# Optimization experiments

Measured on AMD Instinct MI355X. Metric: run time of the kernel, lower is better.

Reference implementation:

```python
import jax, jax.numpy as jnp
import numpy as np

LN_EPS = 1e-5

def _ln(x, gamma, beta):
    mu = jnp.mean(x, axis=-1, keepdims=True)
    var = jnp.mean((x - mu) ** 2, axis=-1, keepdims=True)
    return (x - mu) * jax.lax.rsqrt(var + LN_EPS) * gamma + beta

def setup_inputs() -> dict:
    key = jax.random.key(0)
    ks = jax.random.split(key, 16)
    B, T, D_E, D_H, D_T = 64, 1024, 512, 512, 64
    def xavier(k, shape):
        fan_in, fan_out = shape[0], shape[1]
        a = np.sqrt(6.0 / (fan_in + fan_out))
        return jax.random.uniform(k, shape, jnp.float32, -a, a)
    return {
        "inputs": jax.random.normal(ks[0], (B, T, D_E), jnp.float32),
        "embedding": xavier(ks[1], (D_E, D_H)),
        "w_x_0": xavier(ks[2], (D_H, D_H)),
        "w_h_0": xavier(ks[3], (D_H, D_H)),
        "b_0": xavier(ks[4], (1, D_H)),
        "w_x_1": xavier(ks[5], (D_H, D_H)),
        "w_h_1": xavier(ks[6], (D_H, D_H)),
        "b_1": xavier(ks[7], (1, D_H)),
        "w_x_2": xavier(ks[8], (D_H, D_H)),
        "w_h_2": xavier(ks[9], (D_H, D_H)),
        "b_2": xavier(ks[10], (1, D_H)),
        "ln_gamma": jnp.ones((D_H,), jnp.float32),
        "ln_beta": jnp.zeros((D_H,), jnp.float32),
        "clf_w": xavier(ks[11], (D_H, D_T)),
        "clf_b": jnp.zeros((D_T,), jnp.float32),
    }

def reference(inputs, embedding, w_x_0, w_h_0, b_0, w_x_1, w_h_1, b_1,
              w_x_2, w_h_2, b_2, ln_gamma, ln_beta, clf_w, clf_b):
    B, T, _ = inputs.shape
    D_H = embedding.shape[1]
    # Precompute the (input @ embedding) projection for all steps: [T, B, D_H]
    v_all = jnp.einsum('bte,eh->tbh', inputs, embedding)

    def step(carry, v_t):
        h0p, h1p, h2p, _ = carry
        h0 = jnp.tanh(v_t @ w_x_0 + h0p @ w_h_0 + b_0)
        o0 = _ln(h0, ln_gamma, ln_beta)
        h1 = jnp.tanh(o0 @ w_x_1 + h1p @ w_h_1 + b_1)
        o1 = _ln(h1, ln_gamma, ln_beta)
        h2 = jnp.tanh(o1 @ w_x_2 + h2p @ w_h_2 + b_2)
        o2 = _ln(h2, ln_gamma, ln_beta)
        # note: raw h_t (pre-LayerNorm) is what recurs, per the original code
        return (h0, h1, h2, o2), None

    z = jnp.zeros((B, D_H), inputs.dtype)
    (_, _, _, out_2), _ = jax.lax.scan(step, (z, z, z, z), v_all)
    logits = out_2 @ clf_w + clf_b  # [B, D_T]
    return jax.nn.softmax(logits, axis=1)
```

## Files before the change

kernel.cpp:

```cpp
#include <hip/hip_runtime.h>

#define DH 512
#define TT 1024
#define BB 64
#define DT 64
#define RD 4
#define RG 32

typedef _Float16 f16x8 __attribute__((ext_vector_type(8)));
typedef float f32x4 __attribute__((ext_vector_type(4)));

#define ATILE_HALVES  (64 * 65 * 8)
#define ATILE32_HALVES (64 * 33 * 8)

__device__ __forceinline__ f16x8 cload(const _Float16* p) {
  return *(const volatile f16x8*)p;
}
__device__ __forceinline__ void cstore(_Float16* p, f16x8 v) {
  *(volatile f16x8*)p = v;
}


__global__ __launch_bounds__(512) void eprime_kernel(
    const float* __restrict__ emb, const float* __restrict__ wx0,
    float* __restrict__ Ep)
{
  __shared__ float er[DH];
  const int e = blockIdx.x, j = threadIdx.x;
  er[j] = emb[(size_t)e * DH + j];
  __syncthreads();
  float acc = 0.f;
#pragma unroll 8
  for (int k = 0; k < DH; ++k) acc = fmaf(er[k], wx0[(size_t)k * DH + j], acc);
  Ep[(size_t)e * DH + j] = acc;
}

__global__ __launch_bounds__(512) void pack_kernel(
    const float* __restrict__ Ep, const float* __restrict__ wh0,
    const float* __restrict__ wx1, const float* __restrict__ wh1,
    const float* __restrict__ wx2, const float* __restrict__ wh2,
    const float* __restrict__ gamma, _Float16* __restrict__ dst)
{
  __shared__ float Tt[64][65];
  const int m = blockIdx.z, jt = blockIdx.x, kt = blockIdx.y;
  const float* src = (m == 0) ? Ep : (m == 1) ? wh0 : (m == 2) ? wx1
                   : (m == 3) ? wh1 : (m == 4) ? wx2 : wh2;
  const bool fold = (m == 2 || m == 4);
  const int tx = threadIdx.x & 63, ty = threadIdx.x >> 6;
#pragma unroll
  for (int i = 0; i < 8; ++i) {
    const int k = kt * 64 + ty * 8 + i;
    Tt[ty * 8 + i][tx] = src[(size_t)k * DH + jt * 64 + tx];
  }
  __syncthreads();
#pragma unroll
  for (int i = 0; i < 8; ++i) {
    const int j = jt * 64 + ty * 8 + i;
    const int k = kt * 64 + tx;
    float v = Tt[tx][ty * 8 + i];
    if (fold) v *= gamma[k];
    dst[((size_t)m * DH + j) * DH + k] = (_Float16)v;
  }
}

__global__ __launch_bounds__(512) void fold_kernel(
    const float* __restrict__ b0, const float* __restrict__ b1,
    const float* __restrict__ b2, const float* __restrict__ wx1,
    const float* __restrict__ wx2, const float* __restrict__ gamma,
    const float* __restrict__ beta, const float* __restrict__ clfw,
    const float* __restrict__ clfb,
    float* __restrict__ bfold, float* __restrict__ csum,
    float* __restrict__ clfwf, float* __restrict__ clfbf)
{
  const int j = threadIdx.x;
  if (blockIdx.x == 0) {
    bfold[j] = b0[j];
    float s1 = 0, s2 = 0, c1 = 0, c2 = 0;
    for (int k = 0; k < DH; ++k) {
      const float w1 = wx1[(size_t)k * DH + j], w2 = wx2[(size_t)k * DH + j];
      s1 += beta[k] * w1;  s2 += beta[k] * w2;
      c1 += gamma[k] * w1; c2 += gamma[k] * w2;
    }
    bfold[DH + j] = b1[j] + s1;
    bfold[2 * DH + j] = b2[j] + s2;
    csum[j] = c1; csum[DH + j] = c2;
  } else {
    for (int idx = j; idx < DH * DT; idx += 512) {
      const int k = idx >> 6, d = idx & 63;
      clfwf[idx] = gamma[k] * clfw[(size_t)k * DT + d];
    }
    if (j < DT) {
      float sb = clfb[j];
      for (int k = 0; k < DH; ++k) sb += beta[k] * clfw[(size_t)k * DT + j];
      clfbf[j] = sb;
    }
  }
}

__global__ __launch_bounds__(512, 1) void vgemm_kernel(
    const float* __restrict__ x, const _Float16* __restrict__ Bt,
    _Float16* __restrict__ v)
{
  const int t = blockIdx.x;
  const int tid = threadIdx.x, l = tid & 63, w = tid >> 6;
  __shared__ __align__(16) _Float16 A[ATILE_HALVES];
  {
    const int row = tid >> 3, part = tid & 7;
    const float4* sp = (const float4*)(x + ((size_t)row * TT + t) * DH);
#pragma unroll
    for (int i = 0; i < 8; ++i) {
      const int ks = i * 8 + part;
      const float4 a = sp[ks * 2], b = sp[ks * 2 + 1];
      f16x8 vv;
      vv[0] = (_Float16)a.x; vv[1] = (_Float16)a.y; vv[2] = (_Float16)a.z; vv[3] = (_Float16)a.w;
      vv[4] = (_Float16)b.x; vv[5] = (_Float16)b.y; vv[6] = (_Float16)b.z; vv[7] = (_Float16)b.w;
      *(f16x8*)(A + ((size_t)ks * 65 + row) * 8) = vv;
    }
  }
  __syncthreads();
  const int jb = w * 64;
  const int arowb = l & 15, g = l >> 4;
  f32x4 acc[4][4];
#pragma unroll
  for (int mf = 0; mf < 4; ++mf)
#pragma unroll
    for (int nf = 0; nf < 4; ++nf)
#pragma unroll
      for (int e = 0; e < 4; ++e) acc[mf][nf][e] = 0.f;
#pragma unroll
  for (int kk = 0; kk < 16; ++kk) {
    const int ks = kk * 4 + g;
    f16x8 am[4], bn[4];
#pragma unroll
    for (int mf = 0; mf < 4; ++mf)
      am[mf] = *(const f16x8*)(A + ((size_t)ks * 65 + mf * 16 + arowb) * 8);
#pragma unroll
    for (int nf = 0; nf < 4; ++nf)
      bn[nf] = *(const f16x8*)(Bt + (size_t)(jb + nf * 16 + arowb) * DH + kk * 32 + g * 8);
#pragma unroll
    for (int mf = 0; mf < 4; ++mf)
#pragma unroll
      for (int nf = 0; nf < 4; ++nf)
        acc[mf][nf] = __builtin_amdgcn_mfma_f32_16x16x32_f16(am[mf], bn[nf], acc[mf][nf], 0, 0, 0);
  }
#pragma unroll
  for (int mf = 0; mf < 4; ++mf)
#pragma unroll
    for (int nf = 0; nf < 4; ++nf)
#pragma unroll
      for (int i = 0; i < 4; ++i) {
        const int r = mf * 16 + (l >> 4) * 4 + i;
        const int j = jb + nf * 16 + (l & 15);
        v[((size_t)t * BB + r) * DH + j] = (_Float16)acc[mf][nf][i];
      }
}


__device__ __forceinline__ void stage_h32(_Float16* __restrict__ A,
                                          const _Float16* __restrict__ src64,
                                          int rbase, float* muA, float* rsA,
                                          bool stats, int tid)
{
  const int row = tid >> 4, part = tid & 15;
  const _Float16* sp = src64 + (size_t)(rbase + row) * DH;
  f16x8 v[4];
#pragma unroll
  for (int i = 0; i < 4; ++i) v[i] = cload(sp + (size_t)(i * 16 + part) * 8);
  float sum = 0.f, sq = 0.f;
#pragma unroll
  for (int i = 0; i < 4; ++i) {
    const int ks = i * 16 + part;
    *(f16x8*)(A + ((size_t)ks * 33 + row) * 8) = v[i];
    if (stats) {
#pragma unroll
      for (int e = 0; e < 8; ++e) { const float f = (float)v[i][e]; sum += f; sq += f * f; }
    }
  }
  if (stats) {
    sum += __shfl_xor(sum, 1); sq += __shfl_xor(sq, 1);
    sum += __shfl_xor(sum, 2); sq += __shfl_xor(sq, 2);
    sum += __shfl_xor(sum, 4); sq += __shfl_xor(sq, 4);
    sum += __shfl_xor(sum, 8); sq += __shfl_xor(sq, 8);
    if (part == 0) {
      const float mu = sum * (1.f / DH);
      const float var = sq * (1.f / DH) - mu * mu;
      muA[row] = mu; rsA[row] = rsqrtf(var + 1e-5f);
    }
  }
}

__device__ __forceinline__ void stage_x32(_Float16* __restrict__ A,
                                          const float* __restrict__ inputs,
                                          int rbase, int t, int tid)
{
  const int row = tid >> 4, part = tid & 15;
  const float4* sp = (const float4*)(inputs + ((size_t)(rbase + row) * TT + t) * DH);
#pragma unroll
  for (int i = 0; i < 4; ++i) {
    const int ks = i * 16 + part;
    const float4 a = sp[ks * 2], b = sp[ks * 2 + 1];
    f16x8 vv;
    vv[0] = (_Float16)a.x; vv[1] = (_Float16)a.y; vv[2] = (_Float16)a.z; vv[3] = (_Float16)a.w;
    vv[4] = (_Float16)b.x; vv[5] = (_Float16)b.y; vv[6] = (_Float16)b.z; vv[7] = (_Float16)b.w;
    *(f16x8*)(A + ((size_t)ks * 33 + row) * 8) = vv;
  }
}

__device__ __forceinline__ void stage_h_coh(_Float16* __restrict__ A,
                                            const _Float16* __restrict__ src,
                                            float* muA, float* rsA, bool stats,
                                            int tid)
{
  const int row = tid >> 3, part = tid & 7;
  const _Float16* sp = src + (size_t)row * DH;
  f16x8 v[8];
#pragma unroll
  for (int i = 0; i < 8; ++i) v[i] = cload(sp + (size_t)(i * 8 + part) * 8);
  float sum = 0.f, sq = 0.f;
#pragma unroll
  for (int i = 0; i < 8; ++i) {
    const int ks = i * 8 + part;
    *(f16x8*)(A + ((size_t)ks * 65 + row) * 8) = v[i];
    if (stats) {
#pragma unroll
      for (int e = 0; e < 8; ++e) { const float f = (float)v[i][e]; sum += f; sq += f * f; }
    }
  }
  if (stats) {
    sum += __shfl_xor(sum, 1); sq += __shfl_xor(sq, 1);
    sum += __shfl_xor(sum, 2); sq += __shfl_xor(sq, 2);
    sum += __shfl_xor(sum, 4); sq += __shfl_xor(sq, 4);
    if (part == 0) {
      const float mu = sum * (1.f / DH);
      const float var = sq * (1.f / DH) - mu * mu;
      muA[row] = mu; rsA[row] = rsqrtf(var + 1e-5f);
    }
  }
}

__device__ __forceinline__ void stage_x64(_Float16* __restrict__ A,
                                          const float* __restrict__ inputs,
                                          int t, int tid)
{
  const int row = tid >> 3, part = tid & 7;
  const float4* sp = (const float4*)(inputs + ((size_t)row * TT + t) * DH);
#pragma unroll
  for (int i = 0; i < 8; ++i) {
    const int ks = i * 8 + part;
    const float4 a = sp[ks * 2], b = sp[ks * 2 + 1];
    f16x8 vv;
    vv[0] = (_Float16)a.x; vv[1] = (_Float16)a.y; vv[2] = (_Float16)a.z; vv[3] = (_Float16)a.w;
    vv[4] = (_Float16)b.x; vv[5] = (_Float16)b.y; vv[6] = (_Float16)b.z; vv[7] = (_Float16)b.w;
    *(f16x8*)(A + ((size_t)ks * 65 + row) * 8) = vv;
  }
}

__device__ __forceinline__ void spin_mask(unsigned* p, unsigned tgt) {
  while (true) {
    bool mine = true;
    if (p) mine = (__hip_atomic_load(p, __ATOMIC_RELAXED, __HIP_MEMORY_SCOPE_AGENT) >= tgt);
    if (__all(mine)) break;
    __builtin_amdgcn_s_sleep(1);
  }
}


__global__ __launch_bounds__(512, 1) void rnn12_kernel(
    const float* __restrict__ inputs, const _Float16* __restrict__ v_all,
    const int use_v, const _Float16* __restrict__ packB,
    const float* __restrict__ bfold, const float* __restrict__ csum,
    _Float16* __restrict__ h_base, unsigned* __restrict__ arr)
{
  const int bid = blockIdx.x;
  const int s = bid >> 4, g2 = (bid >> 3) & 1, c = bid & 7;
  const int rbase = g2 * RG;
  const int tid = threadIdx.x;
  const int l = tid & 63, w = tid >> 6;
  const int mg = w >> 2, ng = w & 3;

  __shared__ __align__(16) _Float16 A1[ATILE32_HALVES];
  __shared__ __align__(16) _Float16 A2[ATILE32_HALVES];
  __shared__ __align__(16) _Float16 hout[RG][72];
  __shared__ float muS[RG], rsS[RG];

  const bool sx = (s == 0);
  const bool havev = (use_v != 0);
  const bool needX = (!sx || !havev);

  const int colbase = c * 64 + ng * 16 + (l & 15);
  const int kbase = (l >> 4) * 8;
  f16x8 Bx[16], Bh[16];
  {
    const _Float16* ph = packB + ((size_t)(s * 2 + 1) * DH + colbase) * DH + kbase;
#pragma unroll
    for (int kk = 0; kk < 16; ++kk) Bh[kk] = *(const f16x8*)(ph + kk * 32);
  }
  if (needX) {
    const _Float16* px = packB + ((size_t)(s * 2 + 0) * DH + colbase) * DH + kbase;
#pragma unroll
    for (int kk = 0; kk < 16; ++kk) Bx[kk] = *(const f16x8*)(px + kk * 32);
  }

  const float b_j = bfold[s * DH + colbase];
  const float cs_j = (s > 0) ? csum[(s - 1) * DH + colbase] : 0.f;
  const int g = l >> 4;
  const int fbase = (s * 2 + g2) * 8;
  const int ubase = ((s - 1) * 2 + g2) * 8;

  for (int t = 0; t < TT; ++t) {
    _Float16 vp[4];
    if (sx && havev) {
      const _Float16* vb = v_all + (size_t)t * BB * DH + colbase;
      const int rb = rbase + mg * 16 + (l >> 4) * 4;
#pragma unroll
      for (int i = 0; i < 4; ++i) vp[i] = vb[(size_t)(rb + i) * DH];
    }

    if (w == 0) {
      unsigned* p = nullptr; unsigned tgt = 0;
      if (l < 8 && t >= 1) { p = arr + (fbase + l) * 16; tgt = (unsigned)t; }
      spin_mask(p, tgt);
    }
    __syncthreads();

    if (t >= 1)
      stage_h32(A2, h_base + ((size_t)s * TT + (t - 1)) * BB * DH, rbase,
                nullptr, nullptr, false, tid);
    __syncthreads();

    f32x4 accX, accH;
#pragma unroll
    for (int e = 0; e < 4; ++e) { accX[e] = 0.f; accH[e] = 0.f; }
    const int arow = mg * 16 + (l & 15);
    if (t >= 1) {
#pragma unroll
      for (int kk = 0; kk < 16; ++kk) {
        const int ks = kk * 4 + g;
        const f16x8 aH = *(const f16x8*)(A2 + ((size_t)ks * 33 + arow) * 8);
        accH = __builtin_amdgcn_mfma_f32_16x16x32_f16(aH, Bh[kk], accH, 0, 0, 0);
      }
    }

    if (s > 0) {
      if (w == 0) {
        unsigned* p = (l < 8) ? (arr + (ubase + l) * 16) : nullptr;
        spin_mask(p, (unsigned)(t + 1));
      }
      __syncthreads();
      stage_h32(A1, h_base + ((size_t)(s - 1) * TT + t) * BB * DH, rbase,
                muS, rsS, true, tid);
      __syncthreads();
    } else if (!havev) {
      stage_x32(A1, inputs, rbase, t, tid);
      __syncthreads();
    }

    if (needX) {
#pragma unroll
      for (int kk = 0; kk < 16; ++kk) {
        const int ks = kk * 4 + g;
        const f16x8 aX = *(const f16x8*)(A1 + ((size_t)ks * 33 + arow) * 8);
        accX = __builtin_amdgcn_mfma_f32_16x16x32_f16(aX, Bx[kk], accX, 0, 0, 0);
      }
    }

    const int jl = ng * 16 + (l & 15);
#pragma unroll
    for (int i = 0; i < 4; ++i) {
      const int r = mg * 16 + (l >> 4) * 4 + i;
      float p;
      if (sx) {
        const float v0 = havev ? (float)vp[i] : accX[i];
        p = v0 + accH[i] + b_j;
      } else {
        p = rsS[r] * (accX[i] - muS[r] * cs_j) + accH[i] + b_j;
      }
      hout[r][jl] = (_Float16)tanhf(p);
    }
    __syncthreads();

    if (tid < 256) {
      _Float16* dst = h_base + ((size_t)s * TT + t) * BB * DH;
      const int row = tid >> 3, ch = tid & 7;
      const f16x8 hv = *(const f16x8*)(&hout[row][ch * 8]);
      cstore(dst + (size_t)(rbase + row) * DH + c * 64 + ch * 8, hv);
    }
    __syncthreads();
    if (tid == 0)
      __hip_atomic_store(arr + (fbase + c) * 16, (unsigned)(t + 1),
                         __ATOMIC_RELAXED, __HIP_MEMORY_SCOPE_AGENT);
  }
}


__global__ __launch_bounds__(512, 1) void rnn_ring_kernel(
    const float* __restrict__ inputs, const _Float16* __restrict__ v_all,
    const int use_v, const _Float16* __restrict__ packB,
    const float* __restrict__ bfold, const float* __restrict__ csum,
    _Float16* __restrict__ h_base, unsigned* __restrict__ arr,
    unsigned* __restrict__ cons)
{
  const int bid = blockIdx.x;
  const int s = bid >> 3, c = bid & 7;
  const int tid = threadIdx.x;
  const int l = tid & 63, w = tid >> 6;
  const int mg = w >> 2, ng = w & 3;

  __shared__ __align__(16) _Float16 A1[ATILE_HALVES];
  __shared__ __align__(16) _Float16 A2[ATILE_HALVES];
  __shared__ __align__(16) _Float16 hout[64][72];
  __shared__ float muS[64], rsS[64];

  const bool sx = (s == 0);
  const bool havev = (use_v != 0);
  const bool needX = (!sx || !havev);

  const int colbase = c * 64 + ng * 16 + (l & 15);
  const int kbase = (l >> 4) * 8;
  f16x8 Bx[16], Bh[16];
  {
    const _Float16* ph = packB + ((size_t)(s * 2 + 1) * DH + colbase) * DH + kbase;
#pragma unroll
    for (int kk = 0; kk < 16; ++kk) Bh[kk] = *(const f16x8*)(ph + kk * 32);
  }
  if (needX) {
    const _Float16* px = packB + ((size_t)(s * 2 + 0) * DH + colbase) * DH + kbase;
#pragma unroll
    for (int kk = 0; kk < 16; ++kk) Bx[kk] = *(const f16x8*)(px + kk * 32);
  }

  const float b_j = bfold[s * DH + colbase];
  const float cs_j = (s > 0) ? csum[(s - 1) * DH + colbase] : 0.f;
  const int g = l >> 4;

  for (int t = 0; t < TT; ++t) {
    if (w == 0) {
      unsigned* p = nullptr; unsigned tgt = 0;
      if (l < 8) {
        if (t >= 1) { p = arr + (s * 8 + l) * 16; tgt = (unsigned)t; }
      } else if (l >= 16 && l < 24 && s < 2 && t >= RD) {
        p = cons + (s * 8 + (l - 16)) * 16; tgt = (unsigned)(t - RD + 1);
      }
      spin_mask(p, tgt);
    }
    __syncthreads();
    if (t >= 1)
      stage_h_coh(A2, h_base + (size_t)(s * RD + ((t - 1) & (RD - 1))) * BB * DH,
                  nullptr, nullptr, false, tid);
    __syncthreads();

    f32x4 accX[2], accH[2];
#pragma unroll
    for (int mf = 0; mf < 2; ++mf)
#pragma unroll
      for (int e = 0; e < 4; ++e) { accX[mf][e] = 0.f; accH[mf][e] = 0.f; }

    if (t >= 1) {
#pragma unroll
      for (int kk = 0; kk < 16; ++kk) {
        const int ks = kk * 4 + g;
#pragma unroll
        for (int mf = 0; mf < 2; ++mf) {
          const int arow = mg * 32 + mf * 16 + (l & 15);
          const f16x8 aH = *(const f16x8*)(A2 + ((size_t)ks * 65 + arow) * 8);
          accH[mf] = __builtin_amdgcn_mfma_f32_16x16x32_f16(aH, Bh[kk], accH[mf], 0, 0, 0);
        }
      }
    }

    if (s > 0) {
      if (w == 0) {
        unsigned* p = (l < 8) ? (arr + ((s - 1) * 8 + l) * 16) : nullptr;
        spin_mask(p, (unsigned)(t + 1));
      }
      __syncthreads();
      stage_h_coh(A1, h_base + (size_t)((s - 1) * RD + (t & (RD - 1))) * BB * DH,
                  muS, rsS, true, tid);
      __syncthreads();
      if (tid == 0)
        __hip_atomic_store(cons + ((s - 1) * 8 + c) * 16, (unsigned)(t + 1),
                           __ATOMIC_RELAXED, __HIP_MEMORY_SCOPE_AGENT);
    } else if (!havev) {
      stage_x64(A1, inputs, t, tid);
      __syncthreads();
    }

    if (needX) {
#pragma unroll
      for (int kk = 0; kk < 16; ++kk) {
        const int ks = kk * 4 + g;
#pragma unroll
        for (int mf = 0; mf < 2; ++mf) {
          const int arow = mg * 32 + mf * 16 + (l & 15);
          const f16x8 aX = *(const f16x8*)(A1 + ((size_t)ks * 65 + arow) * 8);
          accX[mf] = __builtin_amdgcn_mfma_f32_16x16x32_f16(aX, Bx[kk], accX[mf], 0, 0, 0);
        }
      }
    }

    const int jl = ng * 16 + (l & 15);
#pragma unroll
    for (int mf = 0; mf < 2; ++mf)
#pragma unroll
      for (int i = 0; i < 4; ++i) {
        const int r = mg * 32 + mf * 16 + (l >> 4) * 4 + i;
        float p;
        if (sx) {
          float v0;
          if (havev) v0 = (float)v_all[((size_t)t * BB + r) * DH + c * 64 + jl];
          else       v0 = accX[mf][i];
          p = v0 + accH[mf][i] + b_j;
        } else {
          p = rsS[r] * (accX[mf][i] - muS[r] * cs_j) + accH[mf][i] + b_j;
        }
        hout[r][jl] = (_Float16)tanhf(p);
      }
    __syncthreads();
    {
      _Float16* dst = h_base + (size_t)(s * RD + (t & (RD - 1))) * BB * DH;
      const int row = tid >> 3, ch = tid & 7;
      const f16x8 hv = *(const f16x8*)(&hout[row][ch * 8]);
      cstore(dst + (size_t)row * DH + c * 64 + ch * 8, hv);
    }
    __syncthreads();
    if (tid == 0)
      __hip_atomic_store(arr + (s * 8 + c) * 16, (unsigned)(t + 1),
                         __ATOMIC_RELAXED, __HIP_MEMORY_SCOPE_AGENT);
  }
}


__global__ __launch_bounds__(64) void clf_kernel(
    const _Float16* __restrict__ h2, const float* __restrict__ clfwf,
    const float* __restrict__ clfbf, float* __restrict__ out)
{
  const int b = blockIdx.x, d = threadIdx.x;
  __shared__ float o2[DH];
  const _Float16* hrow = h2 + (size_t)b * DH;
  float sum = 0.f, sq = 0.f;
#pragma unroll
  for (int i = 0; i < 8; ++i) {
    const float v = (float)hrow[d * 8 + i];
    sum += v; sq += v * v;
  }
#pragma unroll
  for (int off = 32; off; off >>= 1) { sum += __shfl_xor(sum, off); sq += __shfl_xor(sq, off); }
  const float mu = sum * (1.f / DH);
  const float rs = rsqrtf(sq * (1.f / DH) - mu * mu + 1e-5f);
#pragma unroll
  for (int i = 0; i < 8; ++i) o2[d * 8 + i] = ((float)hrow[d * 8 + i] - mu) * rs;
  __syncthreads();
  float acc = clfbf[d];
#pragma unroll 8
  for (int k = 0; k < DH; ++k) acc = fmaf(o2[k], clfwf[k * DT + d], acc);
  float mx = acc;
#pragma unroll
  for (int off = 32; off; off >>= 1) mx = fmaxf(mx, __shfl_xor(mx, off));
  const float e = expf(acc - mx);
  float ss = e;
#pragma unroll
  for (int off = 32; off; off >>= 1) ss += __shfl_xor(ss, off);
  out[(size_t)b * DT + d] = e / ss;
}


extern "C" void kernel_launch(void* const* d_in, const int* in_sizes, int n_in,
                              void* d_out, int out_size, void* d_ws, size_t ws_size,
                              hipStream_t stream) {
  const float* inputs = (const float*)d_in[0];
  const float* emb    = (const float*)d_in[1];
  const float* wx0    = (const float*)d_in[2];
  const float* wh0    = (const float*)d_in[3];
  const float* b0     = (const float*)d_in[4];
  const float* wx1    = (const float*)d_in[5];
  const float* wh1    = (const float*)d_in[6];
  const float* b1     = (const float*)d_in[7];
  const float* wx2    = (const float*)d_in[8];
  const float* wh2    = (const float*)d_in[9];
  const float* b2     = (const float*)d_in[10];
  const float* gamma  = (const float*)d_in[11];
  const float* beta   = (const float*)d_in[12];
  const float* clfw   = (const float*)d_in[13];
  const float* clfb   = (const float*)d_in[14];
  float* out = (float*)d_out;

  char* ws = (char*)d_ws;
  size_t off = 0;
  float*    Ep    = (float*)(ws + off);    off += (size_t)DH * DH * 4;
  _Float16* packB = (_Float16*)(ws + off); off += (size_t)6 * DH * DH * 2;
  float*    bfold = (float*)(ws + off);    off += (size_t)3 * DH * 4;
  float*    csumP = (float*)(ws + off);    off += (size_t)2 * DH * 4;
  float*    clfwf = (float*)(ws + off);    off += (size_t)DH * DT * 4;
  float*    clfbf = (float*)(ws + off);    off += 256;
  unsigned* arr   = (unsigned*)(ws + off); off += (size_t)6 * 8 * 16 * 4;
  unsigned* cons  = (unsigned*)(ws + off); off += (size_t)2 * 8 * 16 * 4;
  off = (off + 255) & ~(size_t)255;
  _Float16* h_base = (_Float16*)(ws + off);

  const size_t uniq_h_bytes = (size_t)3 * TT * BB * DH * 2;
  const size_t ring_h_bytes = (size_t)3 * RD * BB * DH * 2;
  const size_t v_bytes = (size_t)TT * BB * DH * 2;

  const int uniq = (ws_size >= off + uniq_h_bytes) ? 1 : 0;
  const size_t h_bytes = uniq ? uniq_h_bytes : ring_h_bytes;
  size_t off_v = ((off + h_bytes + 255) & ~(size_t)255);
  _Float16* v_all = (_Float16*)(ws + off_v);
  const int use_v = (ws_size >= off_v + v_bytes) ? 1 : 0;

  (void)hipMemsetAsync(arr, 0, (size_t)(6 * 8 * 16 + 2 * 8 * 16) * 4, stream);
  hipLaunchKernelGGL(eprime_kernel, dim3(DH), dim3(512), 0, stream, emb, wx0, Ep);
  hipLaunchKernelGGL(pack_kernel, dim3(8, 8, 6), dim3(512), 0, stream,
                     Ep, wh0, wx1, wh1, wx2, wh2, gamma, packB);
  hipLaunchKernelGGL(fold_kernel, dim3(2), dim3(512), 0, stream,
                     b0, b1, b2, wx1, wx2, gamma, beta, clfw, clfb,
                     bfold, csumP, clfwf, clfbf);
  if (use_v)
    hipLaunchKernelGGL(vgemm_kernel, dim3(TT), dim3(512), 0, stream,
                       inputs, packB, v_all);

  if (uniq)
    hipLaunchKernelGGL(rnn12_kernel, dim3(48), dim3(512), 0, stream,
                       inputs, v_all, use_v, packB, bfold, csumP, h_base, arr);
  else
    hipLaunchKernelGGL(rnn_ring_kernel, dim3(24), dim3(512), 0, stream,
                       inputs, v_all, use_v, packB, bfold, csumP, h_base, arr, cons);

  const _Float16* h2fin = uniq
    ? h_base + ((size_t)2 * TT + (TT - 1)) * BB * DH
    : h_base + (size_t)(2 * RD + ((TT - 1) & (RD - 1))) * BB * DH;
  hipLaunchKernelGGL(clf_kernel, dim3(BB), dim3(DT), 0, stream,
                     h2fin, clfwf, clfbf, out);
}
```

Baseline: 6.594 ms.

## Split recurrent and input projections into separate pipelined block groups

Adds an rnn13 kernel that puts the recurrent h@Wh matmul of each layer on 12 blocks, with weights held in registers and a half-column split. Eight separate producer blocks compute the layer-to-layer input projections (LayerNorm folded into Wx) ahead of time into a new xp buffer, coordinated through flag spinning. This takes the input-projection GEMM off the serial recurrence critical path, and each recurrent block reuses its own freshly computed half of h locally while it waits for the other half. In exchange it needs more workspace for the xp buffer, adds inter-block flag synchronisation, and runs on far fewer blocks (20 instead of 48).

Measured after the change: 12.05 ms. 1.83x slower.

```diff
diff --git a/kernel.cpp b/kernel.cpp
--- a/kernel.cpp
+++ b/kernel.cpp
@@ -10,7 +10,7 @@
 typedef _Float16 f16x8 __attribute__((ext_vector_type(8)));
 typedef float f32x4 __attribute__((ext_vector_type(4)));
 
-#define ATILE_HALVES  (64 * 65 * 8)
+#define ATILE_HALVES   (64 * 65 * 8)
 #define ATILE32_HALVES (64 * 33 * 8)
 
 __device__ __forceinline__ f16x8 cload(const _Float16* p) {
@@ -261,6 +261,221 @@
     if (p) mine = (__hip_atomic_load(p, __ATOMIC_RELAXED, __HIP_MEMORY_SCOPE_AGENT) >= tgt);
     if (__all(mine)) break;
     __builtin_amdgcn_s_sleep(1);
+  }
+}
+
+
+__global__ __launch_bounds__(512, 1) void rnn13_kernel(
+    const _Float16* __restrict__ v_all, const _Float16* __restrict__ packB,
+    const float* __restrict__ bfold, const float* __restrict__ csum,
+    _Float16* __restrict__ h_base, _Float16* __restrict__ xp_base,
+    unsigned* __restrict__ harr, unsigned* __restrict__ xflg)
+{
+  const int bid = blockIdx.x;
+  const int tid = threadIdx.x;
+  const int l = tid & 63, w = tid >> 6;
+  const int g = l >> 4;
+
+  __shared__ __align__(16) _Float16 AT[ATILE32_HALVES];
+  __shared__ __align__(16) _Float16 xpl[32 * 264];
+  __shared__ __align__(16) _Float16 hout[32 * 264];
+  __shared__ float muS[RG], rsS[RG];
+
+  if (bid < 12) {
+    const int s = bid >> 2, rg = (bid >> 1) & 1, half = bid & 1;
+    const int rbase = rg * RG, cbase = half * 256;
+    const int scb = (1 - half) * 256;
+
+    f16x8 Bh[16][2];
+    {
+      const int colb = cbase + w * 32 + (l & 15);
+      const _Float16* pw = packB + ((size_t)(s * 2 + 1) * DH + colb) * DH + (size_t)(l >> 4) * 8;
+#pragma unroll
+      for (int kk = 0; kk < 16; ++kk) {
+        Bh[kk][0] = *(const f16x8*)(pw + kk * 32);
+        Bh[kk][1] = *(const f16x8*)(pw + (size_t)16 * DH + kk * 32);
+      }
+    }
+    const float b0_ = bfold[s * DH + cbase + w * 32 + (l & 15)];
+    const float b1_ = bfold[s * DH + cbase + w * 32 + 16 + (l & 15)];
+    const int sidx = s * 4 + rg * 2 + (1 - half);
+    const int myidx = s * 4 + rg * 2 + half;
+    const int xidx = (s >= 1) ? ((s - 1) * 4 + rg * 2 + half) : -1;
+
+    for (int t = 0; t < TT; ++t) {
+      if (w == 0) {
+        unsigned* p = nullptr; unsigned tgt = 0;
+        if (l == 0 && t >= 1)       { p = harr + (size_t)sidx * 16; tgt = (unsigned)t; }
+        else if (l == 1 && xidx >= 0) { p = xflg + (size_t)xidx * 16; tgt = (unsigned)(t + 1); }
+        spin_mask(p, tgt);
+      }
+      f32x4 acc[2][2];
+#pragma unroll
+      for (int mf = 0; mf < 2; ++mf)
+#pragma unroll
+        for (int e = 0; e < 4; ++e) { acc[mf][0][e] = 0.f; acc[mf][1][e] = 0.f; }
+      if (t >= 1) {
+        const int k0 = half * 8;
+#pragma unroll
+        for (int kq = 0; kq < 8; ++kq) {
+          const int kk = k0 + kq;
+          const int ks = kk * 4 + g;
+#pragma unroll
+          for (int mf = 0; mf < 2; ++mf) {
+            const f16x8 a = *(const f16x8*)(AT + ((size_t)ks * 33 + mf * 16 + (l & 15)) * 8);
+            acc[mf][0] = __builtin_amdgcn_mfma_f32_16x16x32_f16(a, Bh[kk][0], acc[mf][0], 0, 0, 0);
+            acc[mf][1] = __builtin_amdgcn_mfma_f32_16x16x32_f16(a, Bh[kk][1], acc[mf][1], 0, 0, 0);
+          }
+        }
+      }
+      __syncthreads();
+
+      {
+        const int row = tid >> 4, part = tid & 15;
+        if (t >= 1) {
+          const _Float16* sp = h_base + ((size_t)s * TT + (t - 1)) * BB * DH
+                               + (size_t)(rbase + row) * DH + scb + part * 16;
+          const f16x8 v0 = cload(sp), v1 = cload(sp + 8);
+          const int ks0 = (scb >> 3) + part * 2;
+          *(f16x8*)(AT + ((size_t)ks0 * 33 + row) * 8) = v0;
+          *(f16x8*)(AT + ((size_t)(ks0 + 1) * 33 + row) * 8) = v1;
+        }
+        if (s == 0) {
+          const _Float16* xs = v_all + (size_t)t * BB * DH
+                               + (size_t)(rbase + row) * DH + cbase + part * 16;
+          *(f16x8*)(xpl + (size_t)row * 264 + part * 16)     = *(const f16x8*)xs;
+          *(f16x8*)(xpl + (size_t)row * 264 + part * 16 + 8) = *(const f16x8*)(xs + 8);
+        } else {
+          const _Float16* xs = xp_base + ((size_t)(s - 1) * TT + t) * BB * DH
+                               + (size_t)(rbase + row) * DH + cbase + part * 16;
+          *(f16x8*)(xpl + (size_t)row * 264 + part * 16)     = cload(xs);
+          *(f16x8*)(xpl + (size_t)row * 264 + part * 16 + 8) = cload(xs + 8);
+        }
+      }
+      __syncthreads();
+
+      if (t >= 1) {
+        const int k0 = (1 - half) * 8;
+#pragma unroll
+        for (int kq = 0; kq < 8; ++kq) {
+          const int kk = k0 + kq;
+          const int ks = kk * 4 + g;
+#pragma unroll
+          for (int mf = 0; mf < 2; ++mf) {
+            const f16x8 a = *(const f16x8*)(AT + ((size_t)ks * 33 + mf * 16 + (l & 15)) * 8);
+            acc[mf][0] = __builtin_amdgcn_mfma_f32_16x16x32_f16(a, Bh[kk][0], acc[mf][0], 0, 0, 0);
+            acc[mf][1] = __builtin_amdgcn_mfma_f32_16x16x32_f16(a, Bh[kk][1], acc[mf][1], 0, 0, 0);
+          }
+        }
+      }
+
+      {
+        const int coll = w * 32 + (l & 15);
+#pragma unroll
+        for (int mf = 0; mf < 2; ++mf)
+#pragma unroll
+          for (int nf = 0; nf < 2; ++nf)
+#pragma unroll
+            for (int i = 0; i < 4; ++i) {
+              const int r = mf * 16 + g * 4 + i;
+              const int cl = coll + nf * 16;
+              const float p = acc[mf][nf][i] + (float)xpl[(size_t)r * 264 + cl]
+                              + (nf ? b1_ : b0_);
+              const _Float16 hv = (_Float16)tanhf(p);
+              hout[(size_t)r * 264 + cl] = hv;
+              const int kg = cbase + cl;
+              AT[((size_t)(kg >> 3) * 33 + r) * 8 + (kg & 7)] = hv;
+            }
+      }
+      __syncthreads();
+
+      {
+        const int row = tid >> 4, part = tid & 15;
+        _Float16* dst = h_base + ((size_t)s * TT + t) * BB * DH
+                        + (size_t)(rbase + row) * DH + cbase + part * 16;
+        cstore(dst,     *(const f16x8*)(hout + (size_t)row * 264 + part * 16));
+        cstore(dst + 8, *(const f16x8*)(hout + (size_t)row * 264 + part * 16 + 8));
+      }
+      __syncthreads();
+      if (tid == 0)
+        __hip_atomic_store(harr + (size_t)myidx * 16, (unsigned)(t + 1),
+                           __ATOMIC_RELAXED, __HIP_MEMORY_SCOPE_AGENT);
+    }
+  } else {
+    const int e = bid - 12;
+    const int s = 1 + (e >> 2), rg = (e >> 1) & 1, half = e & 1;
+    const int rbase = rg * RG, cbase = half * 256;
+
+    f16x8 Bx[16][2];
+    {
+      const int colb = cbase + w * 32 + (l & 15);
+      const _Float16* pw = packB + ((size_t)(s * 2) * DH + colb) * DH + (size_t)(l >> 4) * 8;
+#pragma unroll
+      for (int kk = 0; kk < 16; ++kk) {
+        Bx[kk][0] = *(const f16x8*)(pw + kk * 32);
+        Bx[kk][1] = *(const f16x8*)(pw + (size_t)16 * DH + kk * 32);
+      }
+    }
+    const float cs0 = csum[(s - 1) * DH + cbase + w * 32 + (l & 15)];
+    const float cs1 = csum[(s - 1) * DH + cbase + w * 32 + 16 + (l & 15)];
+    const int i0 = (s - 1) * 4 + rg * 2 + 0;
+    const int i1 = (s - 1) * 4 + rg * 2 + 1;
+    const int myx = (s - 1) * 4 + rg * 2 + half;
+
+    for (int t = 0; t < TT; ++t) {
+      if (w == 0) {
+        unsigned* p = nullptr; unsigned tgt = 0;
+        if (l == 0)      { p = harr + (size_t)i0 * 16; tgt = (unsigned)(t + 1); }
+        else if (l == 1) { p = harr + (size_t)i1 * 16; tgt = (unsigned)(t + 1); }
+        spin_mask(p, tgt);
+      }
+      __syncthreads();
+      stage_h32(AT, h_base + ((size_t)(s - 1) * TT + t) * BB * DH, rbase,
+                muS, rsS, true, tid);
+      __syncthreads();
+
+      f32x4 acc[2][2];
+#pragma unroll
+      for (int mf = 0; mf < 2; ++mf)
+#pragma unroll
+        for (int ee = 0; ee < 4; ++ee) { acc[mf][0][ee] = 0.f; acc[mf][1][ee] = 0.f; }
+#pragma unroll
+      for (int kk = 0; kk < 16; ++kk) {
+        const int ks = kk * 4 + g;
+#pragma unroll
+        for (int mf = 0; mf < 2; ++mf) {
+          const f16x8 a = *(const f16x8*)(AT + ((size_t)ks * 33 + mf * 16 + (l & 15)) * 8);
+          acc[mf][0] = __builtin_amdgcn_mfma_f32_16x16x32_f16(a, Bx[kk][0], acc[mf][0], 0, 0, 0);
+          acc[mf][1] = __builtin_amdgcn_mfma_f32_16x16x32_f16(a, Bx[kk][1], acc[mf][1], 0, 0, 0);
+        }
+      }
+
+      {
+        const int coll = w * 32 + (l & 15);
+#pragma unroll
+        for (int mf = 0; mf < 2; ++mf)
+#pragma unroll
+          for (int nf = 0; nf < 2; ++nf)
+#pragma unroll
+            for (int i = 0; i < 4; ++i) {
+              const int r = mf * 16 + g * 4 + i;
+              const float val = rsS[r] * (acc[mf][nf][i] - muS[r] * (nf ? cs1 : cs0));
+              hout[(size_t)r * 264 + coll + nf * 16] = (_Float16)val;
+            }
+      }
+      __syncthreads();
+      {
+        const int row = tid >> 4, part = tid & 15;
+        _Float16* dst = xp_base + ((size_t)(s - 1) * TT + t) * BB * DH
+                        + (size_t)(rbase + row) * DH + cbase + part * 16;
+        cstore(dst,     *(const f16x8*)(hout + (size_t)row * 264 + part * 16));
+        cstore(dst + 8, *(const f16x8*)(hout + (size_t)row * 264 + part * 16 + 8));
+      }
+      __syncthreads();
+      if (tid == 0)
+        __hip_atomic_store(xflg + (size_t)myx * 16, (unsigned)(t + 1),
+                           __ATOMIC_RELAXED, __HIP_MEMORY_SCOPE_AGENT);
+    }
   }
 }
 
@@ -592,42 +807,55 @@
   float*    csumP = (float*)(ws + off);    off += (size_t)2 * DH * 4;
   float*    clfwf = (float*)(ws + off);    off += (size_t)DH * DT * 4;
   float*    clfbf = (float*)(ws + off);    off += 256;
-  unsigned* arr   = (unsigned*)(ws + off); off += (size_t)6 * 8 * 16 * 4;
-  unsigned* cons  = (unsigned*)(ws + off); off += (size_t)2 * 8 * 16 * 4;
+  unsigned* flags = (unsigned*)(ws + off); off += (size_t)2048 * 4;
   off = (off + 255) & ~(size_t)255;
   _Float16* h_base = (_Float16*)(ws + off);
 
-  const size_t uniq_h_bytes = (size_t)3 * TT * BB * DH * 2;
+  const size_t H_BYTES  = (size_t)3 * TT * BB * DH * 2;
+  const size_t XP_BYTES = (size_t)2 * TT * BB * DH * 2;
+  const size_t V_BYTES  = (size_t)TT * BB * DH * 2;
   const size_t ring_h_bytes = (size_t)3 * RD * BB * DH * 2;
-  const size_t v_bytes = (size_t)TT * BB * DH * 2;
-
-  const int uniq = (ws_size >= off + uniq_h_bytes) ? 1 : 0;
-  const size_t h_bytes = uniq ? uniq_h_bytes : ring_h_bytes;
-  size_t off_v = ((off + h_bytes + 255) & ~(size_t)255);
-  _Float16* v_all = (_Float16*)(ws + off_v);
-  const int use_v = (ws_size >= off_v + v_bytes) ? 1 : 0;
-
-  (void)hipMemsetAsync(arr, 0, (size_t)(6 * 8 * 16 + 2 * 8 * 16) * 4, stream);
+
+  const int mode13 = (ws_size >= off + H_BYTES + XP_BYTES + V_BYTES) ? 1 : 0;
+  const int mode12 = (!mode13 && ws_size >= off + H_BYTES + V_BYTES) ? 1 : 0;
+
+  (void)hipMemsetAsync(flags, 0, (size_t)2048 * 4, stream);
   hipLaunchKernelGGL(eprime_kernel, dim3(DH), dim3(512), 0, stream, emb, wx0, Ep);
   hipLaunchKernelGGL(pack_kernel, dim3(8, 8, 6), dim3(512), 0, stream,
                      Ep, wh0, wx1, wh1, wx2, wh2, gamma, packB);
   hipLaunchKernelGGL(fold_kernel, dim3(2), dim3(512), 0, stream,
                      b0, b1, b2, wx1, wx2, gamma, beta, clfw, clfb,
                      bfold, csumP, clfwf, clfbf);
-  if (use_v)
+
+  if (mode13) {
+    _Float16* xp_base = (_Float16*)((char*)h_base + H_BYTES);
+    _Float16* v_all   = (_Float16*)((char*)h_base + H_BYTES + XP_BYTES);
+    unsigned* harr = flags;
+    unsigned* xflg = flags + 12 * 16;
     hipLaunchKernelGGL(vgemm_kernel, dim3(TT), dim3(512), 0, stream,
                        inputs, packB, v_all);
-
-  if (uniq)
+    hipLaunchKernelGGL(rnn13_kernel, dim3(20), dim3(512), 0, stream,
+                       v_all, packB, bfold, csumP, h_base, xp_base, harr, xflg);
+    const _Float16* h2fin = h_base + ((size_t)2 * TT + (TT - 1)) * BB * DH;
+    hipLaunchKernelGGL(clf_kernel, dim3(BB), dim3(DT), 0, stream,
+                       h2fin, clfwf, clfbf, out);
+  } else if (mode12) {
+    _Float16* v_all = (_Float16*)((char*)h_base + H_BYTES);
+    hipLaunchKernelGGL(vgemm_kernel, dim3(TT), dim3(512), 0, stream,
+                       inputs, packB, v_all);
     hipLaunchKernelGGL(rnn12_kernel, dim3(48), dim3(512), 0, stream,
-                       inputs, v_all, use_v, packB, bfold, csumP, h_base, arr);
-  else
+                       inputs, v_all, 1, packB, bfold, csumP, h_base, flags);
+    const _Float16* h2fin = h_base + ((size_t)2 * TT + (TT - 1)) * BB * DH;
+    hipLaunchKernelGGL(clf_kernel, dim3(BB), dim3(DT), 0, stream,
+                       h2fin, clfwf, clfbf, out);
+  } else {
+    unsigned* arr  = flags;
+    unsigned* cons = flags + 1024;
+    (void)ring_h_bytes;
     hipLaunchKernelGGL(rnn_ring_kernel, dim3(24), dim3(512), 0, stream,
-                       inputs, v_all, use_v, packB, bfold, csumP, h_base, arr, cons);
-
-  const _Float16* h2fin = uniq
-    ? h_base + ((size_t)2 * TT + (TT - 1)) * BB * DH
-    : h_base + (size_t)(2 * RD + ((TT - 1) & (RD - 1))) * BB * DH;
-  hipLaunchKernelGGL(clf_kernel, dim3(BB), dim3(DT), 0, stream,
-                     h2fin, clfwf, clfbf, out);
-}
+                       inputs, nullptr, 0, packB, bfold, csumP, h_base, arr, cons);
+    const _Float16* h2fin = h_base + (size_t)(2 * RD + ((TT - 1) & (RD - 1))) * BB * DH;
+    hipLaunchKernelGGL(clf_kernel, dim3(BB), dim3(DT), 0, stream,
+                       h2fin, clfwf, clfbf, out);
+  }
+}
```

## Prefetch lower-layer hidden state into registers and fuse LayerNorm stats in new RNN kernel

Applied to the files above, without the earlier changes.

Adds rnn14_kernel, which replaces rnn12 on the path where the workspace is large enough. It loads the previous layer's next-step hidden rows into registers straight after publishing the current step, then writes them to shared memory and computes LayerNorm mean and variance in the same pass. This is meant to overlap the cross-layer dependency wait and global loads with other work and to cut a separate staging pass. The workspace flag layout is also simplified and the ring fallback no longer uses v_all. The trade-off is more register pressure and an extra wait on the lower-layer flag inside each step.

Result: faster. 6.088 ms (-7.7%).

```diff
diff --git a/kernel.cpp b/kernel.cpp
--- a/kernel.cpp
+++ b/kernel.cpp
@@ -10,7 +10,7 @@
 typedef _Float16 f16x8 __attribute__((ext_vector_type(8)));
 typedef float f32x4 __attribute__((ext_vector_type(4)));
 
-#define ATILE_HALVES  (64 * 65 * 8)
+#define ATILE_HALVES   (64 * 65 * 8)
 #define ATILE32_HALVES (64 * 33 * 8)
 
 __device__ __forceinline__ f16x8 cload(const _Float16* p) {
@@ -261,6 +261,167 @@
     if (p) mine = (__hip_atomic_load(p, __ATOMIC_RELAXED, __HIP_MEMORY_SCOPE_AGENT) >= tgt);
     if (__all(mine)) break;
     __builtin_amdgcn_s_sleep(1);
+  }
+}
+
+
+__global__ __launch_bounds__(512, 1) void rnn14_kernel(
+    const float* __restrict__ inputs, const _Float16* __restrict__ v_all,
+    const int use_v, const _Float16* __restrict__ packB,
+    const float* __restrict__ bfold, const float* __restrict__ csum,
+    _Float16* __restrict__ h_base, unsigned* __restrict__ arr)
+{
+  const int bid = blockIdx.x;
+  const int s = bid >> 4, g2 = (bid >> 3) & 1, c = bid & 7;
+  const int rbase = g2 * RG;
+  const int tid = threadIdx.x;
+  const int l = tid & 63, w = tid >> 6;
+  const int mg = w >> 2, ng = w & 3;
+  const int row16 = tid >> 4, part16 = tid & 15;
+
+  __shared__ __align__(16) _Float16 A1[ATILE32_HALVES];
+  __shared__ __align__(16) _Float16 A2[ATILE32_HALVES];
+  __shared__ __align__(16) _Float16 hout[RG][72];
+  __shared__ float muS[RG], rsS[RG];
+
+  const bool sx = (s == 0);
+  const bool havev = (use_v != 0);
+  const bool needX = (!sx || !havev);
+
+  const int colbase = c * 64 + ng * 16 + (l & 15);
+  const int kbase = (l >> 4) * 8;
+  f16x8 Bx[16], Bh[16];
+  {
+    const _Float16* ph = packB + ((size_t)(s * 2 + 1) * DH + colbase) * DH + kbase;
+#pragma unroll
+    for (int kk = 0; kk < 16; ++kk) Bh[kk] = *(const f16x8*)(ph + kk * 32);
+  }
+  if (needX) {
+    const _Float16* px = packB + ((size_t)(s * 2 + 0) * DH + colbase) * DH + kbase;
+#pragma unroll
+    for (int kk = 0; kk < 16; ++kk) Bx[kk] = *(const f16x8*)(px + kk * 32);
+  }
+
+  const float b_j = bfold[s * DH + colbase];
+  const float cs_j = (s > 0) ? csum[(s - 1) * DH + colbase] : 0.f;
+  const int g = l >> 4;
+  const int fbase = (s * 2 + g2) * 8;
+  const int ubase = ((s - 1) * 2 + g2) * 8;
+
+  f16x8 a1r[4];
+  if (s > 0) {
+    if (w == 0) {
+      unsigned* p = (l < 8) ? (arr + (ubase + l) * 16) : nullptr;
+      spin_mask(p, 1u);
+    }
+    __syncthreads();
+    const _Float16* sp = h_base + ((size_t)(s - 1) * TT) * BB * DH
+                         + (size_t)(rbase + row16) * DH;
+#pragma unroll
+    for (int i = 0; i < 4; ++i) a1r[i] = cload(sp + (size_t)(i * 16 + part16) * 8);
+  }
+
+  for (int t = 0; t < TT; ++t) {
+    if (s > 0) {
+      float sum = 0.f, sq = 0.f;
+#pragma unroll
+      for (int i = 0; i < 4; ++i) {
+        const int ks = i * 16 + part16;
+        *(f16x8*)(A1 + ((size_t)ks * 33 + row16) * 8) = a1r[i];
+#pragma unroll
+        for (int e = 0; e < 8; ++e) { const float f = (float)a1r[i][e]; sum += f; sq += f * f; }
+      }
+      sum += __shfl_xor(sum, 1); sq += __shfl_xor(sq, 1);
+      sum += __shfl_xor(sum, 2); sq += __shfl_xor(sq, 2);
+      sum += __shfl_xor(sum, 4); sq += __shfl_xor(sq, 4);
+      sum += __shfl_xor(sum, 8); sq += __shfl_xor(sq, 8);
+      if (part16 == 0) {
+        const float mu = sum * (1.f / DH);
+        const float var = sq * (1.f / DH) - mu * mu;
+        muS[row16] = mu; rsS[row16] = rsqrtf(var + 1e-5f);
+      }
+    }
+
+    _Float16 vp[4];
+    if (sx && havev) {
+      const _Float16* vb = v_all + (size_t)t * BB * DH + colbase;
+      const int rb = rbase + mg * 16 + (l >> 4) * 4;
+#pragma unroll
+      for (int i = 0; i < 4; ++i) vp[i] = vb[(size_t)(rb + i) * DH];
+    } else if (sx && !havev) {
+      stage_x32(A1, inputs, rbase, t, tid);
+    }
+
+    if (w == 0) {
+      unsigned* p = nullptr; unsigned tgt = 0;
+      if (l < 8 && t >= 1) { p = arr + (fbase + l) * 16; tgt = (unsigned)t; }
+      spin_mask(p, tgt);
+    }
+    __syncthreads();
+
+    if (t >= 1)
+      stage_h32(A2, h_base + ((size_t)s * TT + (t - 1)) * BB * DH, rbase,
+                nullptr, nullptr, false, tid);
+    __syncthreads();
+
+    f32x4 accX, accH;
+#pragma unroll
+    for (int e = 0; e < 4; ++e) { accX[e] = 0.f; accH[e] = 0.f; }
+    const int arow = mg * 16 + (l & 15);
+    if (t >= 1) {
+#pragma unroll
+      for (int kk = 0; kk < 16; ++kk) {
+        const int ks = kk * 4 + g;
+        const f16x8 aH = *(const f16x8*)(A2 + ((size_t)ks * 33 + arow) * 8);
+        accH = __builtin_amdgcn_mfma_f32_16x16x32_f16(aH, Bh[kk], accH, 0, 0, 0);
+      }
+    }
+    if (needX) {
+#pragma unroll
+      for (int kk = 0; kk < 16; ++kk) {
+        const int ks = kk * 4 + g;
+        const f16x8 aX = *(const f16x8*)(A1 + ((size_t)ks * 33 + arow) * 8);
+        accX = __builtin_amdgcn_mfma_f32_16x16x32_f16(aX, Bx[kk], accX, 0, 0, 0);
+      }
+    }
+
+    const int jl = ng * 16 + (l & 15);
+#pragma unroll
+    for (int i = 0; i < 4; ++i) {
+      const int r = mg * 16 + (l >> 4) * 4 + i;
+      float p;
+      if (sx) {
+        const float v0 = havev ? (float)vp[i] : accX[i];
+        p = v0 + accH[i] + b_j;
+      } else {
+        p = rsS[r] * (accX[i] - muS[r] * cs_j) + accH[i] + b_j;
+      }
+      hout[r][jl] = (_Float16)tanhf(p);
+    }
+    __syncthreads();
+
+    if (tid < 256) {
+      _Float16* dst = h_base + ((size_t)s * TT + t) * BB * DH;
+      const int row = tid >> 3, ch = tid & 7;
+      const f16x8 hv = *(const f16x8*)(&hout[row][ch * 8]);
+      cstore(dst + (size_t)(rbase + row) * DH + c * 64 + ch * 8, hv);
+    }
+    __syncthreads();
+    if (tid == 0)
+      __hip_atomic_store(arr + (fbase + c) * 16, (unsigned)(t + 1),
+                         __ATOMIC_RELAXED, __HIP_MEMORY_SCOPE_AGENT);
+
+    if (s > 0 && t + 1 < TT) {
+      if (w == 0) {
+        unsigned* p = (l < 8) ? (arr + (ubase + l) * 16) : nullptr;
+        spin_mask(p, (unsigned)(t + 2));
+      }
+      __syncthreads();
+      const _Float16* sp = h_base + ((size_t)(s - 1) * TT + (t + 1)) * BB * DH
+                           + (size_t)(rbase + row16) * DH;
+#pragma unroll
+      for (int i = 0; i < 4; ++i) a1r[i] = cload(sp + (size_t)(i * 16 + part16) * 8);
+    }
   }
 }
 
@@ -592,42 +753,39 @@
   float*    csumP = (float*)(ws + off);    off += (size_t)2 * DH * 4;
   float*    clfwf = (float*)(ws + off);    off += (size_t)DH * DT * 4;
   float*    clfbf = (float*)(ws + off);    off += 256;
-  unsigned* arr   = (unsigned*)(ws + off); off += (size_t)6 * 8 * 16 * 4;
-  unsigned* cons  = (unsigned*)(ws + off); off += (size_t)2 * 8 * 16 * 4;
+  unsigned* flags = (unsigned*)(ws + off); off += (size_t)2048 * 4;
   off = (off + 255) & ~(size_t)255;
   _Float16* h_base = (_Float16*)(ws + off);
 
-  const size_t uniq_h_bytes = (size_t)3 * TT * BB * DH * 2;
-  const size_t ring_h_bytes = (size_t)3 * RD * BB * DH * 2;
-  const size_t v_bytes = (size_t)TT * BB * DH * 2;
-
-  const int uniq = (ws_size >= off + uniq_h_bytes) ? 1 : 0;
-  const size_t h_bytes = uniq ? uniq_h_bytes : ring_h_bytes;
-  size_t off_v = ((off + h_bytes + 255) & ~(size_t)255);
-  _Float16* v_all = (_Float16*)(ws + off_v);
-  const int use_v = (ws_size >= off_v + v_bytes) ? 1 : 0;
-
-  (void)hipMemsetAsync(arr, 0, (size_t)(6 * 8 * 16 + 2 * 8 * 16) * 4, stream);
+  const size_t H_BYTES = (size_t)3 * TT * BB * DH * 2;
+  const size_t V_BYTES = (size_t)TT * BB * DH * 2;
+
+  const int uniq = (ws_size >= off + H_BYTES + V_BYTES) ? 1 : 0;
+
+  (void)hipMemsetAsync(flags, 0, (size_t)2048 * 4, stream);
   hipLaunchKernelGGL(eprime_kernel, dim3(DH), dim3(512), 0, stream, emb, wx0, Ep);
   hipLaunchKernelGGL(pack_kernel, dim3(8, 8, 6), dim3(512), 0, stream,
                      Ep, wh0, wx1, wh1, wx2, wh2, gamma, packB);
   hipLaunchKernelGGL(fold_kernel, dim3(2), dim3(512), 0, stream,
                      b0, b1, b2, wx1, wx2, gamma, beta, clfw, clfb,
                      bfold, csumP, clfwf, clfbf);
-  if (use_v)
+
+  if (uniq) {
+    _Float16* v_all = (_Float16*)((char*)h_base + H_BYTES);
     hipLaunchKernelGGL(vgemm_kernel, dim3(TT), dim3(512), 0, stream,
                        inputs, packB, v_all);
-
-  if (uniq)
-    hipLaunchKernelGGL(rnn12_kernel, dim3(48), dim3(512), 0, stream,
-                       inputs, v_all, use_v, packB, bfold, csumP, h_base, arr);
-  else
+    hipLaunchKernelGGL(rnn14_kernel, dim3(48), dim3(512), 0, stream,
+                       inputs, v_all, 1, packB, bfold, csumP, h_base, flags);
+    const _Float16* h2fin = h_base + ((size_t)2 * TT + (TT - 1)) * BB * DH;
+    hipLaunchKernelGGL(clf_kernel, dim3(BB), dim3(DT), 0, stream,
+                       h2fin, clfwf, clfbf, out);
+  } else {
+    unsigned* arr  = flags;
+    unsigned* cons = flags + 1024;
     hipLaunchKernelGGL(rnn_ring_kernel, dim3(24), dim3(512), 0, stream,
-                       inputs, v_all, use_v, packB, bfold, csumP, h_base, arr, cons);
-
-  const _Float16* h2fin = uniq
-    ? h_base + ((size_t)2 * TT + (TT - 1)) * BB * DH
-    : h_base + (size_t)(2 * RD + ((TT - 1) & (RD - 1))) * BB * DH;
-  hipLaunchKernelGGL(clf_kernel, dim3(BB), dim3(DT), 0, stream,
-                     h2fin, clfwf, clfbf, out);
-}
+                       inputs, nullptr, 0, packB, bfold, csumP, h_base, arr, cons);
+    const _Float16* h2fin = h_base + (size_t)(2 * RD + ((TT - 1) & (RD - 1))) * BB * DH;
+    hipLaunchKernelGGL(clf_kernel, dim3(BB), dim3(DT), 0, stream,
+                       h2fin, clfwf, clfbf, out);
+  }
+}
```

## Prefetch next-layer input into registers and overlap h staging with X MFMAs

Applied to the files above, without the earlier changes.

In the per-layer RNN kernel, the lower layer's h for step t+1 is now loaded into registers at the end of step t, right after its readiness spin. LayerNorm statistics are computed from those registers while writing them to shared memory. The own-layer h(t-1) tile is also loaded into registers and written to shared memory after the X-side MFMAs, which removes one staging pass and several barriers from the critical path. This moves the upstream-layer wait earlier and raises register pressure. The host code also merges the flag buffers and only takes the unique-history path when both the h and v buffers fit.

Result: faster. 5.950 ms (-9.8%).

```diff
diff --git a/kernel.cpp b/kernel.cpp
--- a/kernel.cpp
+++ b/kernel.cpp
@@ -10,7 +10,7 @@
 typedef _Float16 f16x8 __attribute__((ext_vector_type(8)));
 typedef float f32x4 __attribute__((ext_vector_type(4)));
 
-#define ATILE_HALVES  (64 * 65 * 8)
+#define ATILE_HALVES   (64 * 65 * 8)
 #define ATILE32_HALVES (64 * 33 * 8)
 
 __device__ __forceinline__ f16x8 cload(const _Float16* p) {
@@ -265,7 +265,7 @@
 }
 
 
-__global__ __launch_bounds__(512, 1) void rnn12_kernel(
+__global__ __launch_bounds__(512, 1) void rnn15_kernel(
     const float* __restrict__ inputs, const _Float16* __restrict__ v_all,
     const int use_v, const _Float16* __restrict__ packB,
     const float* __restrict__ bfold, const float* __restrict__ csum,
@@ -277,6 +277,7 @@
   const int tid = threadIdx.x;
   const int l = tid & 63, w = tid >> 6;
   const int mg = w >> 2, ng = w & 3;
+  const int row16 = tid >> 4, part16 = tid & 15;
 
   __shared__ __align__(16) _Float16 A1[ATILE32_HALVES];
   __shared__ __align__(16) _Float16 A2[ATILE32_HALVES];
@@ -307,13 +308,48 @@
   const int fbase = (s * 2 + g2) * 8;
   const int ubase = ((s - 1) * 2 + g2) * 8;
 
+  f16x8 a1r[4];
+  if (s > 0) {
+    if (w == 0) {
+      unsigned* p = (l < 8) ? (arr + (ubase + l) * 16) : nullptr;
+      spin_mask(p, 1u);
+    }
+    __syncthreads();
+    const _Float16* sp = h_base + ((size_t)(s - 1) * TT) * BB * DH
+                         + (size_t)(rbase + row16) * DH;
+#pragma unroll
+    for (int i = 0; i < 4; ++i) a1r[i] = cload(sp + (size_t)(i * 16 + part16) * 8);
+  }
+
   for (int t = 0; t < TT; ++t) {
+    if (s > 0) {
+      float sum = 0.f, sq = 0.f;
+#pragma unroll
+      for (int i = 0; i < 4; ++i) {
+        const int ks = i * 16 + part16;
+        *(f16x8*)(A1 + ((size_t)ks * 33 + row16) * 8) = a1r[i];
+#pragma unroll
+        for (int e = 0; e < 8; ++e) { const float f = (float)a1r[i][e]; sum += f; sq += f * f; }
+      }
+      sum += __shfl_xor(sum, 1); sq += __shfl_xor(sq, 1);
+      sum += __shfl_xor(sum, 2); sq += __shfl_xor(sq, 2);
+      sum += __shfl_xor(sum, 4); sq += __shfl_xor(sq, 4);
+      sum += __shfl_xor(sum, 8); sq += __shfl_xor(sq, 8);
+      if (part16 == 0) {
+        const float mu = sum * (1.f / DH);
+        const float var = sq * (1.f / DH) - mu * mu;
+        muS[row16] = mu; rsS[row16] = rsqrtf(var + 1e-5f);
+      }
+    }
+
     _Float16 vp[4];
     if (sx && havev) {
       const _Float16* vb = v_all + (size_t)t * BB * DH + colbase;
       const int rb = rbase + mg * 16 + (l >> 4) * 4;
 #pragma unroll
       for (int i = 0; i < 4; ++i) vp[i] = vb[(size_t)(rb + i) * DH];
+    } else if (sx && !havev) {
+      stage_x32(A1, inputs, rbase, t, tid);
     }
 
     if (w == 0) {
@@ -323,44 +359,40 @@
     }
     __syncthreads();
 
-    if (t >= 1)
-      stage_h32(A2, h_base + ((size_t)s * TT + (t - 1)) * BB * DH, rbase,
-                nullptr, nullptr, false, tid);
-    __syncthreads();
+    f16x8 a2r[4];
+    if (t >= 1) {
+      const _Float16* sp = h_base + ((size_t)s * TT + (t - 1)) * BB * DH
+                           + (size_t)(rbase + row16) * DH;
+#pragma unroll
+      for (int i = 0; i < 4; ++i) a2r[i] = cload(sp + (size_t)(i * 16 + part16) * 8);
+    }
 
     f32x4 accX, accH;
 #pragma unroll
     for (int e = 0; e < 4; ++e) { accX[e] = 0.f; accH[e] = 0.f; }
     const int arow = mg * 16 + (l & 15);
+    if (needX) {
+#pragma unroll
+      for (int kk = 0; kk < 16; ++kk) {
+        const int ks = kk * 4 + g;
+        const f16x8 aX = *(const f16x8*)(A1 + ((size_t)ks * 33 + arow) * 8);
+        accX = __builtin_amdgcn_mfma_f32_16x16x32_f16(aX, Bx[kk], accX, 0, 0, 0);
+      }
+    }
+
+    if (t >= 1) {
+#pragma unroll
+      for (int i = 0; i < 4; ++i)
+        *(f16x8*)(A2 + ((size_t)(i * 16 + part16) * 33 + row16) * 8) = a2r[i];
+    }
+    __syncthreads();
+
     if (t >= 1) {
 #pragma unroll
       for (int kk = 0; kk < 16; ++kk) {
         const int ks = kk * 4 + g;
         const f16x8 aH = *(const f16x8*)(A2 + ((size_t)ks * 33 + arow) * 8);
         accH = __builtin_amdgcn_mfma_f32_16x16x32_f16(aH, Bh[kk], accH, 0, 0, 0);
-      }
-    }
-
-    if (s > 0) {
-      if (w == 0) {
-        unsigned* p = (l < 8) ? (arr + (ubase + l) * 16) : nullptr;
-        spin_mask(p, (unsigned)(t + 1));
-      }
-      __syncthreads();
-      stage_h32(A1, h_base + ((size_t)(s - 1) * TT + t) * BB * DH, rbase,
-                muS, rsS, true, tid);
-      __syncthreads();
-    } else if (!havev) {
-      stage_x32(A1, inputs, rbase, t, tid);
-      __syncthreads();
-    }
-
-    if (needX) {
-#pragma unroll
-      for (int kk = 0; kk < 16; ++kk) {
-        const int ks = kk * 4 + g;
-        const f16x8 aX = *(const f16x8*)(A1 + ((size_t)ks * 33 + arow) * 8);
-        accX = __builtin_amdgcn_mfma_f32_16x16x32_f16(aX, Bx[kk], accX, 0, 0, 0);
       }
     }
 
@@ -385,10 +417,23 @@
       const f16x8 hv = *(const f16x8*)(&hout[row][ch * 8]);
       cstore(dst + (size_t)(rbase + row) * DH + c * 64 + ch * 8, hv);
     }
+    if (s > 0 && t + 1 < TT) {
+      if (w == 0) {
+        unsigned* p = (l < 8) ? (arr + (ubase + l) * 16) : nullptr;
+        spin_mask(p, (unsigned)(t + 2));
+      }
+    }
     __syncthreads();
     if (tid == 0)
       __hip_atomic_store(arr + (fbase + c) * 16, (unsigned)(t + 1),
                          __ATOMIC_RELAXED, __HIP_MEMORY_SCOPE_AGENT);
+
+    if (s > 0 && t + 1 < TT) {
+      const _Float16* sp = h_base + ((size_t)(s - 1) * TT + (t + 1)) * BB * DH
+                           + (size_t)(rbase + row16) * DH;
+#pragma unroll
+      for (int i = 0; i < 4; ++i) a1r[i] = cload(sp + (size_t)(i * 16 + part16) * 8);
+    }
   }
 }
 
@@ -592,42 +637,39 @@
   float*    csumP = (float*)(ws + off);    off += (size_t)2 * DH * 4;
   float*    clfwf = (float*)(ws + off);    off += (size_t)DH * DT * 4;
   float*    clfbf = (float*)(ws + off);    off += 256;
-  unsigned* arr   = (unsigned*)(ws + off); off += (size_t)6 * 8 * 16 * 4;
-  unsigned* cons  = (unsigned*)(ws + off); off += (size_t)2 * 8 * 16 * 4;
+  unsigned* flags = (unsigned*)(ws + off); off += (size_t)2048 * 4;
   off = (off + 255) & ~(size_t)255;
   _Float16* h_base = (_Float16*)(ws + off);
 
-  const size_t uniq_h_bytes = (size_t)3 * TT * BB * DH * 2;
-  const size_t ring_h_bytes = (size_t)3 * RD * BB * DH * 2;
-  const size_t v_bytes = (size_t)TT * BB * DH * 2;
-
-  const int uniq = (ws_size >= off + uniq_h_bytes) ? 1 : 0;
-  const size_t h_bytes = uniq ? uniq_h_bytes : ring_h_bytes;
-  size_t off_v = ((off + h_bytes + 255) & ~(size_t)255);
-  _Float16* v_all = (_Float16*)(ws + off_v);
-  const int use_v = (ws_size >= off_v + v_bytes) ? 1 : 0;
-
-  (void)hipMemsetAsync(arr, 0, (size_t)(6 * 8 * 16 + 2 * 8 * 16) * 4, stream);
+  const size_t H_BYTES = (size_t)3 * TT * BB * DH * 2;
+  const size_t V_BYTES = (size_t)TT * BB * DH * 2;
+
+  const int uniq = (ws_size >= off + H_BYTES + V_BYTES) ? 1 : 0;
+
+  (void)hipMemsetAsync(flags, 0, (size_t)2048 * 4, stream);
   hipLaunchKernelGGL(eprime_kernel, dim3(DH), dim3(512), 0, stream, emb, wx0, Ep);
   hipLaunchKernelGGL(pack_kernel, dim3(8, 8, 6), dim3(512), 0, stream,
                      Ep, wh0, wx1, wh1, wx2, wh2, gamma, packB);
   hipLaunchKernelGGL(fold_kernel, dim3(2), dim3(512), 0, stream,
                      b0, b1, b2, wx1, wx2, gamma, beta, clfw, clfb,
                      bfold, csumP, clfwf, clfbf);
-  if (use_v)
+
+  if (uniq) {
+    _Float16* v_all = (_Float16*)((char*)h_base + H_BYTES);
     hipLaunchKernelGGL(vgemm_kernel, dim3(TT), dim3(512), 0, stream,
                        inputs, packB, v_all);
-
-  if (uniq)
-    hipLaunchKernelGGL(rnn12_kernel, dim3(48), dim3(512), 0, stream,
-                       inputs, v_all, use_v, packB, bfold, csumP, h_base, arr);
-  else
+    hipLaunchKernelGGL(rnn15_kernel, dim3(48), dim3(512), 0, stream,
+                       inputs, v_all, 1, packB, bfold, csumP, h_base, flags);
+    const _Float16* h2fin = h_base + ((size_t)2 * TT + (TT - 1)) * BB * DH;
+    hipLaunchKernelGGL(clf_kernel, dim3(BB), dim3(DT), 0, stream,
+                       h2fin, clfwf, clfbf, out);
+  } else {
+    unsigned* arr  = flags;
+    unsigned* cons = flags + 1024;
     hipLaunchKernelGGL(rnn_ring_kernel, dim3(24), dim3(512), 0, stream,
-                       inputs, v_all, use_v, packB, bfold, csumP, h_base, arr, cons);
-
-  const _Float16* h2fin = uniq
-    ? h_base + ((size_t)2 * TT + (TT - 1)) * BB * DH
-    : h_base + (size_t)(2 * RD + ((TT - 1) & (RD - 1))) * BB * DH;
-  hipLaunchKernelGGL(clf_kernel, dim3(BB), dim3(DT), 0, stream,
-                     h2fin, clfwf, clfbf, out);
-}
+                       inputs, nullptr, 0, packB, bfold, csumP, h_base, arr, cons);
+    const _Float16* h2fin = h_base + (size_t)(2 * RD + ((TT - 1) & (RD - 1))) * BB * DH;
+    hipLaunchKernelGGL(clf_kernel, dim3(BB), dim3(DT), 0, stream,
+                       h2fin, clfwf, clfbf, out);
+  }
+}
```
